# Optimization experiments

Measured on AMD Instinct MI355X. Metric: run time of the kernel, lower is better.

The kernel has to match this reference:

```python
import jax, jax.numpy as jnp
import numpy as np

B, C, O, H, W = 4, 64, 64, 128, 128
KH = KW = 3
K = KH * KW  # 9 kernel positions
MRM = 10.0   # max_residue_magnitude


def setup_inputs() -> dict:
    key = jax.random.key(0)
    ks = jax.random.split(key, 6)
    return {
        "x_main": jax.random.normal(ks[0], (B, C, H, W), jnp.float32),
        "x_extra": jax.random.normal(ks[1], (B, C, H, W), jnp.float32),
        "pre_offset": jax.random.normal(ks[2], (B, K, H, W, 2), jnp.float32) * 2.0,
        "pre_sim": jax.random.uniform(ks[3], (B, K, H, W), jnp.float32),
        "weight": jax.random.normal(ks[4], (O, C, KH, KW), jnp.float32) / np.sqrt(C * K),
        "bias": jnp.zeros((O,), jnp.float32),
        "w_om": jax.random.normal(ks[5], (3 * K, C, KH, KW), jnp.float32) * 0.01,
        "b_om": jnp.zeros((3 * K,), jnp.float32),
    }


def _bilinear(img, py, px):
    """img: [C,Hi,Wi]; py, px: [K,Ho,Wo] float sample coords. Zero padding outside."""
    Hi, Wi = img.shape[1], img.shape[2]
    y0 = jnp.floor(py)
    x0 = jnp.floor(px)
    dy = py - y0  # [K,Ho,Wo]
    dx = px - x0

    def gather(yi, xi):
        valid = ((yi >= 0) & (yi <= Hi - 1) & (xi >= 0) & (xi <= Wi - 1)).astype(img.dtype)
        yc = jnp.clip(yi, 0, Hi - 1).astype(jnp.int32)
        xc = jnp.clip(xi, 0, Wi - 1).astype(jnp.int32)
        return img[:, yc, xc] * valid[None]  # [C,K,Ho,Wo]

    v00 = gather(y0, x0)
    v01 = gather(y0, x0 + 1)
    v10 = gather(y0 + 1, x0)
    v11 = gather(y0 + 1, x0 + 1)
    return (v00 * (1 - dy) * (1 - dx) + v01 * (1 - dy) * dx
            + v10 * dy * (1 - dx) + v11 * dy * dx)


def reference(x_main, x_extra, pre_offset, pre_sim, weight, bias, w_om, b_om):
    # conv_offset_mask: 3x3, stride 1, pad 1 -> [B, 3K, H, W]
    out = jax.lax.conv_general_dilated(
        x_extra, w_om, (1, 1), ((1, 1), (1, 1)),
        dimension_numbers=("NCHW", "OIHW", "NCHW")) + b_om[None, :, None, None]
    o1, o2, mask = jnp.split(out, 3, axis=1)  # each [B,K,H,W]
    offset = MRM * jnp.tanh(jnp.concatenate([o1, o2], axis=1))  # [B,2K,H,W]
    # pre_offset reorder: even channels <- pre_offset[...,1] (y), odd <- pre_offset[...,0] (x)
    off_y = offset[:, 0::2] + pre_offset[..., 1]  # [B,K,H,W]
    off_x = offset[:, 1::2] + pre_offset[..., 0]
    mask = jax.nn.sigmoid(mask * pre_sim)  # use_sim=True

    f32 = offset.dtype
    ky = (jnp.arange(K) // KW).astype(f32)  # kernel row per position k
    kx = (jnp.arange(K) % KW).astype(f32)   # kernel col per position k
    # base grid: p = out_pos*stride - pad + k*dil = h - 1 + ky (stride=1,pad=1,dil=1)
    py = off_y + (jnp.arange(H, dtype=f32)[None, None, :, None] - 1.0) + ky[None, :, None, None]
    px = off_x + (jnp.arange(W, dtype=f32)[None, None, None, :] - 1.0) + kx[None, :, None, None]

    sampled = jax.vmap(_bilinear)(x_main, py, px)      # [B,C,K,H,W]
    sampled = sampled * mask[:, None]                   # modulated (DCNv2)
    y = jnp.einsum("bckhw,ock->bohw", sampled, weight.reshape(O, C, K))
    return y + bias[None, :, None, None]
```

## Files before the change

kernel.cpp:

```cpp
#include <hip/hip_runtime.h>
#include <math.h>

#define Bn 4
#define Cn 64
#define On 64
#define Hn 128
#define Wn 128
#define Kn 9
#define HWn (Hn*Wn)
#define ZROW 16384
#define XBSTRIDE (16385*64)

typedef short v8s __attribute__((ext_vector_type(8)));
typedef _Float16 v8h __attribute__((ext_vector_type(8)));
typedef float v4f __attribute__((ext_vector_type(4)));

__device__ inline unsigned short f2bf(float f) {
  unsigned u = __builtin_bit_cast(unsigned, f);
  u += 0x7fff + ((u >> 16) & 1);
  return (unsigned short)(u >> 16);
}
__device__ inline float bf2f(unsigned short h) {
  unsigned u = ((unsigned)h) << 16;
  return __builtin_bit_cast(float, u);
}
__device__ inline unsigned short f2h(float f) {
  _Float16 h = (_Float16)f;
  return __builtin_bit_cast(unsigned short, h);
}
__device__ inline float h2f(unsigned v) {
  _Float16 h = __builtin_bit_cast(_Float16, (unsigned short)(v & 0xffff));
  return (float)h;
}

__global__ __launch_bounds__(256) void k_prep(
    const float* __restrict__ x_main,
    const float* __restrict__ x_extra,
    const float* __restrict__ weight,
    const float* __restrict__ w_om,
    unsigned short* __restrict__ xT,
    _Float16* __restrict__ xeF,
    unsigned short* __restrict__ Wfrag,
    _Float16* __restrict__ WOMfrag)
{
  const int blk = blockIdx.x;
  const int t = threadIdx.x;
  const int lane = t & 63;
  const int grp = t >> 6;

  if (blk < 2048) {
    __shared__ float tile[64 * 65];
    int isExtra = blk >> 10;
    int b  = (blk >> 8) & 3;
    int p0 = (blk & 255) << 6;
    const float* src = (isExtra ? x_extra : x_main) + b * Cn * HWn + p0;
    #pragma unroll
    for (int i = 0; i < 16; ++i) {
      int c = i * 4 + grp;
      tile[c * 65 + lane] = src[c * HWn + lane];
    }
    __syncthreads();
    if (!isExtra) {
      unsigned short* dst = xT + b * XBSTRIDE + p0 * 64;
      #pragma unroll
      for (int i = 0; i < 16; ++i) {
        int p = i * 4 + grp;
        dst[p * 64 + lane] = f2bf(tile[lane * 65 + p]);
      }
    } else {
      _Float16* dst = xeF + b * XBSTRIDE + p0 * 64;
      #pragma unroll
      for (int i = 0; i < 16; ++i) {
        int p = i * 4 + grp;
        dst[p * 64 + lane] = (_Float16)tile[lane * 65 + p];
      }
    }
  } else {
    int rb = blk - 2048;
    for (int idx = rb * 256 + t; idx < 36864; idx += 64 * 256) {
      int j  = idx & 7;
      int ln = (idx >> 3) & 63;
      int hk = (idx >> 9) & 1;
      int ot = (idx >> 10) & 3;
      int k  = idx >> 12;
      int o = ot * 16 + (ln & 15);
      int c = hk * 32 + (ln >> 4) * 8 + j;
      Wfrag[idx] = f2bf(weight[(o * Cn + c) * Kn + k]);
    }
    for (int idx = rb * 256 + t; idx < 18432; idx += 64 * 256) {
      int j    = idx & 7;
      int ln   = (idx >> 3) & 63;
      int jt   = (idx >> 9) & 1;
      int half = (idx >> 10) & 1;
      int k9   = idx >> 11;
      int jo = jt * 16 + (ln & 15);
      int c  = half * 32 + (ln >> 4) * 8 + j;
      float v = (jo < 27) ? w_om[(jo * Cn + c) * Kn + k9] : 0.f;
      WOMfrag[idx] = (_Float16)v;
    }
    if (rb == 0 && t < 256) {
      int b = t >> 6, c = t & 63;
      xT[b * XBSTRIDE + ZROW * 64 + c] = 0;
      xeF[b * XBSTRIDE + ZROW * 64 + c] = (_Float16)0.f;
    }
  }
}

__global__ __launch_bounds__(256, 4) void k_fused(
    const unsigned short* __restrict__ xT,
    const _Float16* __restrict__ xeF,
    const unsigned short* __restrict__ Wfrag,
    const _Float16* __restrict__ WOMfrag,
    const float* __restrict__ pre_offset,
    const float* __restrict__ pre_sim,
    const float* __restrict__ b_om,
    const float* __restrict__ bias,
    float* __restrict__ out)
{
  __shared__ float jbuf[4 * 16 * 36];
  __shared__ uint4 recbuf[4 * 16 * 9];

  const int t    = threadIdx.x;
  const int lane = t & 63;
  const int wv   = __builtin_amdgcn_readfirstlane(t >> 6);
  const int blk  = blockIdx.x;
  const int b    = blk >> 8;
  const int h    = (blk >> 1) & 127;
  const int wq   = (blk & 1) * 4 + wv;
  const int kq   = lane >> 4;
  const int n    = lane & 15;
  const int w    = wq * 16 + n;

  unsigned tapoff[9];
  #pragma unroll
  for (int k9 = 0; k9 < 9; ++k9) {
    int r  = h - 1 + k9 / 3;
    int cc = w - 1 + k9 % 3;
    bool v = ((unsigned)r < (unsigned)Hn) & ((unsigned)cc < (unsigned)Wn);
    tapoff[k9] = (v ? (unsigned)(r * Wn + cc) : (unsigned)ZROW) * 64u;
  }

  const _Float16* xe = xeF + b * XBSTRIDE;
  const v8h* Wom = (const v8h*)WOMfrag;
  v4f ca0 = {0,0,0,0}, ca1 = {0,0,0,0};
  for (int k9 = 0; k9 < 9; ++k9) {
    #pragma unroll
    for (int half = 0; half < 2; ++half) {
      int abase = ((k9 * 2 + half) * 2) * 64 + lane;
      v8h A0 = Wom[abase];
      v8h A1 = Wom[abase + 64];
      v8h Bt = *(const v8h*)(xe + tapoff[k9] + half * 32 + kq * 8);
      ca0 = __builtin_amdgcn_mfma_f32_16x16x32_f16(A0, Bt, ca0, 0, 0, 0);
      ca1 = __builtin_amdgcn_mfma_f32_16x16x32_f16(A1, Bt, ca1, 0, 0, 0);
    }
  }

  float* jb = jbuf + wv * (16 * 36);
  *(v4f*)(jb + n * 36 + kq * 4)      = ca0;
  *(v4f*)(jb + n * 36 + 16 + kq * 4) = ca1;

  uint4* rb = recbuf + wv * (16 * 9);
  if (kq < 3) {
    #pragma unroll
    for (int kk = 0; kk < 3; ++kk) {
      int k = kq * 3 + kk;
      float sy = jb[n * 36 + 2 * k]     + b_om[2 * k];
      float sx = jb[n * 36 + 2 * k + 1] + b_om[2 * k + 1];
      float sm = jb[n * 36 + 18 + k]    + b_om[18 + k];
      int pbase = ((b * Kn + k) * Hn + h) * Wn + w;
      float2 po = *(const float2*)(pre_offset + pbase * 2);
      float py = 10.f * tanhf(sy) + po.y + (float)(h - 1 + k / 3);
      float px = 10.f * tanhf(sx) + po.x + (float)(w - 1 + k % 3);
      float m  = 1.f / (1.f + expf(-sm * pre_sim[pbase]));
      float fy = floorf(py), fx = floorf(px);
      float dy = py - fy, dx = px - fx;
      int y0 = (int)fy, x0 = (int)fx;
      int y1 = y0 + 1, x1 = x0 + 1;
      bool vy0 = (y0 >= 0) & (y0 < Hn), vy1 = (y1 >= 0) & (y1 < Hn);
      bool vx0 = (x0 >= 0) & (x0 < Wn), vx1 = (x1 >= 0) & (x1 < Wn);
      unsigned r00 = (vy0 & vx0) ? (unsigned)(y0 * Wn + x0) : ZROW;
      unsigned r01 = (vy0 & vx1) ? (unsigned)(y0 * Wn + x1) : ZROW;
      unsigned r10 = (vy1 & vx0) ? (unsigned)(y1 * Wn + x0) : ZROW;
      unsigned r11 = (vy1 & vx1) ? (unsigned)(y1 * Wn + x1) : ZROW;
      float wy0 = 1.f - dy, wx0 = 1.f - dx;
      uint4 rec;
      rec.x = r00 | (r01 << 16);
      rec.y = r10 | (r11 << 16);
      rec.z = (unsigned)f2h(wy0 * wx0 * m) | ((unsigned)f2h(wy0 * dx * m) << 16);
      rec.w = (unsigned)f2h(dy * wx0 * m) | ((unsigned)f2h(dy * dx * m) << 16);
      rb[n * 9 + k] = rec;
    }
  }

  v4f acc0 = {0,0,0,0}, acc1 = {0,0,0,0}, acc2 = {0,0,0,0}, acc3 = {0,0,0,0};
  const unsigned short* xb = xT + b * XBSTRIDE;
  const v8s* Wf = (const v8s*)Wfrag;

  uint4 rec0   = rb[n * 9 + 0];
  uint4 rec_nx = rb[n * 9 + 1];
  float w00 = h2f(rec0.z), w01 = h2f(rec0.z >> 16);
  float w10 = h2f(rec0.w), w11 = h2f(rec0.w >> 16);
  unsigned o00 = (rec0.x & 0xffff) * 64 + kq * 8;
  unsigned o01 = (rec0.x >> 16)    * 64 + kq * 8;
  unsigned o10 = (rec0.y & 0xffff) * 64 + kq * 8;
  unsigned o11 = (rec0.y >> 16)    * 64 + kq * 8;
  v8s C0 = *(const v8s*)(xb + o00);
  v8s C1 = *(const v8s*)(xb + o01);
  v8s C2 = *(const v8s*)(xb + o10);
  v8s C3 = *(const v8s*)(xb + o11);

  #pragma unroll
  for (int k = 0; k < 9; ++k) {
    v8s H0 = *(const v8s*)(xb + o00 + 32);
    v8s H1 = *(const v8s*)(xb + o01 + 32);
    v8s H2 = *(const v8s*)(xb + o10 + 32);
    v8s H3 = *(const v8s*)(xb + o11 + 32);

    v8s N0, N1, N2, N3;
    float nw00 = 0.f, nw01 = 0.f, nw10 = 0.f, nw11 = 0.f;
    unsigned p00 = 0, p01 = 0, p10 = 0, p11 = 0;
    if (k < 8) {
      nw00 = h2f(rec_nx.z); nw01 = h2f(rec_nx.z >> 16);
      nw10 = h2f(rec_nx.w); nw11 = h2f(rec_nx.w >> 16);
      p00 = (rec_nx.x & 0xffff) * 64 + kq * 8;
      p01 = (rec_nx.x >> 16)    * 64 + kq * 8;
      p10 = (rec_nx.y & 0xffff) * 64 + kq * 8;
      p11 = (rec_nx.y >> 16)    * 64 + kq * 8;
      N0 = *(const v8s*)(xb + p00);
      N1 = *(const v8s*)(xb + p01);
      N2 = *(const v8s*)(xb + p10);
      N3 = *(const v8s*)(xb + p11);
    }
    uint4 rec_nx2 = rec_nx;
    if (k < 7) rec_nx2 = rb[n * 9 + k + 2];

    __builtin_amdgcn_sched_barrier(0);

    const v8s* wk = Wf + (k * 8) * 64 + lane;
    v8s A0 = wk[0 * 64], A1 = wk[1 * 64], A2 = wk[2 * 64], A3 = wk[3 * 64];
    v8s A4 = wk[4 * 64], A5 = wk[5 * 64], A6 = wk[6 * 64], A7 = wk[7 * 64];

    v8s Bf0, Bf1;
    #pragma unroll
    for (int j = 0; j < 8; ++j) {
      float s = fmaf(bf2f((unsigned short)C0[j]), w00,
                fmaf(bf2f((unsigned short)C1[j]), w01,
                fmaf(bf2f((unsigned short)C2[j]), w10,
                     bf2f((unsigned short)C3[j]) * w11)));
      Bf0[j] = (short)f2bf(s);
    }
    #pragma unroll
    for (int j = 0; j < 8; ++j) {
      float s = fmaf(bf2f((unsigned short)H0[j]), w00,
                fmaf(bf2f((unsigned short)H1[j]), w01,
                fmaf(bf2f((unsigned short)H2[j]), w10,
                     bf2f((unsigned short)H3[j]) * w11)));
      Bf1[j] = (short)f2bf(s);
    }

    acc0 = __builtin_amdgcn_mfma_f32_16x16x32_bf16(A0, Bf0, acc0, 0, 0, 0);
    acc1 = __builtin_amdgcn_mfma_f32_16x16x32_bf16(A2, Bf0, acc1, 0, 0, 0);
    acc2 = __builtin_amdgcn_mfma_f32_16x16x32_bf16(A4, Bf0, acc2, 0, 0, 0);
    acc3 = __builtin_amdgcn_mfma_f32_16x16x32_bf16(A6, Bf0, acc3, 0, 0, 0);
    acc0 = __builtin_amdgcn_mfma_f32_16x16x32_bf16(A1, Bf1, acc0, 0, 0, 0);
    acc1 = __builtin_amdgcn_mfma_f32_16x16x32_bf16(A3, Bf1, acc1, 0, 0, 0);
    acc2 = __builtin_amdgcn_mfma_f32_16x16x32_bf16(A5, Bf1, acc2, 0, 0, 0);
    acc3 = __builtin_amdgcn_mfma_f32_16x16x32_bf16(A7, Bf1, acc3, 0, 0, 0);

    if (k < 8) {
      C0 = N0; C1 = N1; C2 = N2; C3 = N3;
      w00 = nw00; w01 = nw01; w10 = nw10; w11 = nw11;
      o00 = p00; o01 = p01; o10 = p10; o11 = p11;
      rec_nx = rec_nx2;
    }
  }

  const float4* b4 = (const float4*)bias;
  float4 vb0 = b4[0 * 4 + kq], vb1 = b4[1 * 4 + kq];
  float4 vb2 = b4[2 * 4 + kq], vb3 = b4[3 * 4 + kq];
  float* ob = out + (b * On) * HWn + h * Wn + wq * 16 + n;
  #pragma unroll
  for (int reg = 0; reg < 4; ++reg) {
    ob[(0 * 16 + kq * 4 + reg) * HWn] = acc0[reg] + ((const float*)&vb0)[reg];
    ob[(1 * 16 + kq * 4 + reg) * HWn] = acc1[reg] + ((const float*)&vb1)[reg];
    ob[(2 * 16 + kq * 4 + reg) * HWn] = acc2[reg] + ((const float*)&vb2)[reg];
    ob[(3 * 16 + kq * 4 + reg) * HWn] = acc3[reg] + ((const float*)&vb3)[reg];
  }
}

extern "C" void kernel_launch(void* const* d_in, const int* in_sizes, int n_in,
                              void* d_out, int out_size, void* d_ws, size_t ws_size,
                              hipStream_t stream) {
  const float* x_main     = (const float*)d_in[0];
  const float* x_extra    = (const float*)d_in[1];
  const float* pre_offset = (const float*)d_in[2];
  const float* pre_sim    = (const float*)d_in[3];
  const float* weight     = (const float*)d_in[4];
  const float* bias       = (const float*)d_in[5];
  const float* w_om       = (const float*)d_in[6];
  const float* b_om       = (const float*)d_in[7];
  float* out = (float*)d_out;

  char* ws = (char*)d_ws;
  unsigned short* xT      = (unsigned short*)(ws);
  _Float16*       xeF     = (_Float16*)(ws + 8389120);
  unsigned short* Wfrag   = (unsigned short*)(ws + 16778240);
  _Float16*       WOMfrag = (_Float16*)(ws + 16851968);

  k_prep<<<2112, 256, 0, stream>>>(x_main, x_extra, weight, w_om,
                                   xT, xeF, Wfrag, WOMfrag);
  k_fused<<<1024, 256, 0, stream>>>(xT, xeF, Wfrag, WOMfrag,
                                    pre_offset, pre_sim, b_om, bias, out);
}
```

Baseline: 150.0 us.

## Switch deformable sampling to fp16 packed math, vectorize prep, remap blocks

```diff
diff --git a/kernel.cpp b/kernel.cpp
--- a/kernel.cpp
+++ b/kernel.cpp
@@ -11,42 +11,31 @@
 #define ZROW 16384
 #define XBSTRIDE (16385*64)
 
-typedef short v8s __attribute__((ext_vector_type(8)));
 typedef _Float16 v8h __attribute__((ext_vector_type(8)));
+typedef _Float16 v2h __attribute__((ext_vector_type(2)));
 typedef float v4f __attribute__((ext_vector_type(4)));
 
-__device__ inline unsigned short f2bf(float f) {
-  unsigned u = __builtin_bit_cast(unsigned, f);
-  u += 0x7fff + ((u >> 16) & 1);
-  return (unsigned short)(u >> 16);
-}
-__device__ inline float bf2f(unsigned short h) {
-  unsigned u = ((unsigned)h) << 16;
-  return __builtin_bit_cast(float, u);
-}
 __device__ inline unsigned short f2h(float f) {
   _Float16 h = (_Float16)f;
   return __builtin_bit_cast(unsigned short, h);
 }
-__device__ inline float h2f(unsigned v) {
-  _Float16 h = __builtin_bit_cast(_Float16, (unsigned short)(v & 0xffff));
-  return (float)h;
-}
+__device__ inline _Float16 u2h(unsigned v) {
+  return __builtin_bit_cast(_Float16, (unsigned short)(v & 0xffff));
+}
+__device__ inline v8h sp8(_Float16 x) { v8h v = {x,x,x,x,x,x,x,x}; return v; }
 
 __global__ __launch_bounds__(256) void k_prep(
     const float* __restrict__ x_main,
     const float* __restrict__ x_extra,
     const float* __restrict__ weight,
     const float* __restrict__ w_om,
-    unsigned short* __restrict__ xT,
+    _Float16* __restrict__ xT,
     _Float16* __restrict__ xeF,
-    unsigned short* __restrict__ Wfrag,
+    _Float16* __restrict__ Wfrag,
     _Float16* __restrict__ WOMfrag)
 {
   const int blk = blockIdx.x;
   const int t = threadIdx.x;
-  const int lane = t & 63;
-  const int grp = t >> 6;
 
   if (blk < 2048) {
     __shared__ float tile[64 * 65];
@@ -55,25 +44,23 @@
     int p0 = (blk & 255) << 6;
     const float* src = (isExtra ? x_extra : x_main) + b * Cn * HWn + p0;
     #pragma unroll
-    for (int i = 0; i < 16; ++i) {
-      int c = i * 4 + grp;
-      tile[c * 65 + lane] = src[c * HWn + lane];
+    for (int i = 0; i < 4; ++i) {
+      int c  = i * 16 + (t >> 4);
+      int p4 = (t & 15) * 4;
+      float4 v = *(const float4*)(src + c * HWn + p4);
+      tile[c * 65 + p4 + 0] = v.x;
+      tile[c * 65 + p4 + 1] = v.y;
+      tile[c * 65 + p4 + 2] = v.z;
+      tile[c * 65 + p4 + 3] = v.w;
     }
     __syncthreads();
-    if (!isExtra) {
-      unsigned short* dst = xT + b * XBSTRIDE + p0 * 64;
-      #pragma unroll
-      for (int i = 0; i < 16; ++i) {
-        int p = i * 4 + grp;
-        dst[p * 64 + lane] = f2bf(tile[lane * 65 + p]);
-      }
-    } else {
-      _Float16* dst = xeF + b * XBSTRIDE + p0 * 64;
-      #pragma unroll
-      for (int i = 0; i < 16; ++i) {
-        int p = i * 4 + grp;
-        dst[p * 64 + lane] = (_Float16)tile[lane * 65 + p];
-      }
+    _Float16* dst = (isExtra ? xeF : xT) + b * XBSTRIDE + p0 * 64;
+    #pragma unroll
+    for (int i = 0; i < 8; ++i) {
+      int p  = i * 8 + (t >> 5);
+      int c2 = (t & 31) * 2;
+      v2h pk = { (_Float16)tile[c2 * 65 + p], (_Float16)tile[(c2 + 1) * 65 + p] };
+      *(v2h*)(dst + p * 64 + c2) = pk;
     }
   } else {
     int rb = blk - 2048;
@@ -85,7 +72,7 @@
       int k  = idx >> 12;
       int o = ot * 16 + (ln & 15);
       int c = hk * 32 + (ln >> 4) * 8 + j;
-      Wfrag[idx] = f2bf(weight[(o * Cn + c) * Kn + k]);
+      Wfrag[idx] = (_Float16)weight[(o * Cn + c) * Kn + k];
     }
     for (int idx = rb * 256 + t; idx < 18432; idx += 64 * 256) {
       int j    = idx & 7;
@@ -100,16 +87,16 @@
     }
     if (rb == 0 && t < 256) {
       int b = t >> 6, c = t & 63;
-      xT[b * XBSTRIDE + ZROW * 64 + c] = 0;
+      xT[b * XBSTRIDE + ZROW * 64 + c] = (_Float16)0.f;
       xeF[b * XBSTRIDE + ZROW * 64 + c] = (_Float16)0.f;
     }
   }
 }
 
 __global__ __launch_bounds__(256, 4) void k_fused(
-    const unsigned short* __restrict__ xT,
+    const _Float16* __restrict__ xT,
     const _Float16* __restrict__ xeF,
-    const unsigned short* __restrict__ Wfrag,
+    const _Float16* __restrict__ Wfrag,
     const _Float16* __restrict__ WOMfrag,
     const float* __restrict__ pre_offset,
     const float* __restrict__ pre_sim,
@@ -123,7 +110,8 @@
   const int t    = threadIdx.x;
   const int lane = t & 63;
   const int wv   = __builtin_amdgcn_readfirstlane(t >> 6);
-  const int blk  = blockIdx.x;
+  const int raw  = blockIdx.x;
+  const int blk  = ((raw & 7) << 7) | (raw >> 3);
   const int b    = blk >> 8;
   const int h    = (blk >> 1) & 127;
   const int wq   = (blk & 1) * 4 + wv;
@@ -169,9 +157,11 @@
       float sm = jb[n * 36 + 18 + k]    + b_om[18 + k];
       int pbase = ((b * Kn + k) * Hn + h) * Wn + w;
       float2 po = *(const float2*)(pre_offset + pbase * 2);
-      float py = 10.f * tanhf(sy) + po.y + (float)(h - 1 + k / 3);
-      float px = 10.f * tanhf(sx) + po.x + (float)(w - 1 + k % 3);
-      float m  = 1.f / (1.f + expf(-sm * pre_sim[pbase]));
+      float ey = __expf(2.f * sy);
+      float ex = __expf(2.f * sx);
+      float py = 10.f - 20.f / (ey + 1.f) + po.y + (float)(h - 1 + k / 3);
+      float px = 10.f - 20.f / (ex + 1.f) + po.x + (float)(w - 1 + k % 3);
+      float m  = 1.f / (1.f + __expf(-sm * pre_sim[pbase]));
       float fy = floorf(py), fx = floorf(px);
       float dy = py - fy, dx = px - fx;
       int y0 = (int)fy, x0 = (int)fx;
@@ -193,84 +183,64 @@
   }
 
   v4f acc0 = {0,0,0,0}, acc1 = {0,0,0,0}, acc2 = {0,0,0,0}, acc3 = {0,0,0,0};
-  const unsigned short* xb = xT + b * XBSTRIDE;
-  const v8s* Wf = (const v8s*)Wfrag;
+  const _Float16* xb = xT + b * XBSTRIDE;
+  const v8h* Wf = (const v8h*)Wfrag;
 
   uint4 rec0   = rb[n * 9 + 0];
   uint4 rec_nx = rb[n * 9 + 1];
-  float w00 = h2f(rec0.z), w01 = h2f(rec0.z >> 16);
-  float w10 = h2f(rec0.w), w11 = h2f(rec0.w >> 16);
-  unsigned o00 = (rec0.x & 0xffff) * 64 + kq * 8;
-  unsigned o01 = (rec0.x >> 16)    * 64 + kq * 8;
-  unsigned o10 = (rec0.y & 0xffff) * 64 + kq * 8;
-  unsigned o11 = (rec0.y >> 16)    * 64 + kq * 8;
-  v8s C0 = *(const v8s*)(xb + o00);
-  v8s C1 = *(const v8s*)(xb + o01);
-  v8s C2 = *(const v8s*)(xb + o10);
-  v8s C3 = *(const v8s*)(xb + o11);
+  _Float16 h00 = u2h(rec0.z), h01 = u2h(rec0.z >> 16);
+  _Float16 h10 = u2h(rec0.w), h11 = u2h(rec0.w >> 16);
+  unsigned o00 = (rec0.x & 0xffff) * 64u + kq * 8;
+  unsigned o01 = (rec0.x >> 16)    * 64u + kq * 8;
+  unsigned o10 = (rec0.y & 0xffff) * 64u + kq * 8;
+  unsigned o11 = (rec0.y >> 16)    * 64u + kq * 8;
+  v8h C0 = *(const v8h*)(xb + o00), D0 = *(const v8h*)(xb + o00 + 32);
+  v8h C1 = *(const v8h*)(xb + o01), D1 = *(const v8h*)(xb + o01 + 32);
+  v8h C2 = *(const v8h*)(xb + o10), D2 = *(const v8h*)(xb + o10 + 32);
+  v8h C3 = *(const v8h*)(xb + o11), D3 = *(const v8h*)(xb + o11 + 32);
 
   #pragma unroll
   for (int k = 0; k < 9; ++k) {
-    v8s H0 = *(const v8s*)(xb + o00 + 32);
-    v8s H1 = *(const v8s*)(xb + o01 + 32);
-    v8s H2 = *(const v8s*)(xb + o10 + 32);
-    v8s H3 = *(const v8s*)(xb + o11 + 32);
-
-    v8s N0, N1, N2, N3;
-    float nw00 = 0.f, nw01 = 0.f, nw10 = 0.f, nw11 = 0.f;
-    unsigned p00 = 0, p01 = 0, p10 = 0, p11 = 0;
+    v8h N0, N1, N2, N3, M0, M1, M2, M3;
+    _Float16 nh00 = (_Float16)0.f, nh01 = (_Float16)0.f;
+    _Float16 nh10 = (_Float16)0.f, nh11 = (_Float16)0.f;
     if (k < 8) {
-      nw00 = h2f(rec_nx.z); nw01 = h2f(rec_nx.z >> 16);
-      nw10 = h2f(rec_nx.w); nw11 = h2f(rec_nx.w >> 16);
-      p00 = (rec_nx.x & 0xffff) * 64 + kq * 8;
-      p01 = (rec_nx.x >> 16)    * 64 + kq * 8;
-      p10 = (rec_nx.y & 0xffff) * 64 + kq * 8;
-      p11 = (rec_nx.y >> 16)    * 64 + kq * 8;
-      N0 = *(const v8s*)(xb + p00);
-      N1 = *(const v8s*)(xb + p01);
-      N2 = *(const v8s*)(xb + p10);
-      N3 = *(const v8s*)(xb + p11);
+      nh00 = u2h(rec_nx.z); nh01 = u2h(rec_nx.z >> 16);
+      nh10 = u2h(rec_nx.w); nh11 = u2h(rec_nx.w >> 16);
+      unsigned p00 = (rec_nx.x & 0xffff) * 64u + kq * 8;
+      unsigned p01 = (rec_nx.x >> 16)    * 64u + kq * 8;
+      unsigned p10 = (rec_nx.y & 0xffff) * 64u + kq * 8;
+      unsigned p11 = (rec_nx.y >> 16)    * 64u + kq * 8;
+      N0 = *(const v8h*)(xb + p00); M0 = *(const v8h*)(xb + p00 + 32);
+      N1 = *(const v8h*)(xb + p01); M1 = *(const v8h*)(xb + p01 + 32);
+      N2 = *(const v8h*)(xb + p10); M2 = *(const v8h*)(xb + p10 + 32);
+      N3 = *(const v8h*)(xb + p11); M3 = *(const v8h*)(xb + p11 + 32);
     }
     uint4 rec_nx2 = rec_nx;
     if (k < 7) rec_nx2 = rb[n * 9 + k + 2];
 
     __builtin_amdgcn_sched_barrier(0);
 
-    const v8s* wk = Wf + (k * 8) * 64 + lane;
-    v8s A0 = wk[0 * 64], A1 = wk[1 * 64], A2 = wk[2 * 64], A3 = wk[3 * 64];
-    v8s A4 = wk[4 * 64], A5 = wk[5 * 64], A6 = wk[6 * 64], A7 = wk[7 * 64];
-
-    v8s Bf0, Bf1;
-    #pragma unroll
-    for (int j = 0; j < 8; ++j) {
-      float s = fmaf(bf2f((unsigned short)C0[j]), w00,
-                fmaf(bf2f((unsigned short)C1[j]), w01,
-                fmaf(bf2f((unsigned short)C2[j]), w10,
-                     bf2f((unsigned short)C3[j]) * w11)));
-      Bf0[j] = (short)f2bf(s);
-    }
-    #pragma unroll
-    for (int j = 0; j < 8; ++j) {
-      float s = fmaf(bf2f((unsigned short)H0[j]), w00,
-                fmaf(bf2f((unsigned short)H1[j]), w01,
-                fmaf(bf2f((unsigned short)H2[j]), w10,
-                     bf2f((unsigned short)H3[j]) * w11)));
-      Bf1[j] = (short)f2bf(s);
-    }
-
-    acc0 = __builtin_amdgcn_mfma_f32_16x16x32_bf16(A0, Bf0, acc0, 0, 0, 0);
-    acc1 = __builtin_amdgcn_mfma_f32_16x16x32_bf16(A2, Bf0, acc1, 0, 0, 0);
-    acc2 = __builtin_amdgcn_mfma_f32_16x16x32_bf16(A4, Bf0, acc2, 0, 0, 0);
-    acc3 = __builtin_amdgcn_mfma_f32_16x16x32_bf16(A6, Bf0, acc3, 0, 0, 0);
-    acc0 = __builtin_amdgcn_mfma_f32_16x16x32_bf16(A1, Bf1, acc0, 0, 0, 0);
-    acc1 = __builtin_amdgcn_mfma_f32_16x16x32_bf16(A3, Bf1, acc1, 0, 0, 0);
-    acc2 = __builtin_amdgcn_mfma_f32_16x16x32_bf16(A5, Bf1, acc2, 0, 0, 0);
-    acc3 = __builtin_amdgcn_mfma_f32_16x16x32_bf16(A7, Bf1, acc3, 0, 0, 0);
+    const v8h* wk = Wf + (k * 8) * 64 + lane;
+    v8h A0 = wk[0 * 64], A1 = wk[1 * 64], A2 = wk[2 * 64], A3 = wk[3 * 64];
+    v8h A4 = wk[4 * 64], A5 = wk[5 * 64], A6 = wk[6 * 64], A7 = wk[7 * 64];
+
+    v8h Bf0 = C0 * sp8(h00) + C1 * sp8(h01) + C2 * sp8(h10) + C3 * sp8(h11);
+    v8h Bf1 = D0 * sp8(h00) + D1 * sp8(h01) + D2 * sp8(h10) + D3 * sp8(h11);
+
+    acc0 = __builtin_amdgcn_mfma_f32_16x16x32_f16(A0, Bf0, acc0, 0, 0, 0);
+    acc1 = __builtin_amdgcn_mfma_f32_16x16x32_f16(A2, Bf0, acc1, 0, 0, 0);
+    acc2 = __builtin_amdgcn_mfma_f32_16x16x32_f16(A4, Bf0, acc2, 0, 0, 0);
+    acc3 = __builtin_amdgcn_mfma_f32_16x16x32_f16(A6, Bf0, acc3, 0, 0, 0);
+    acc0 = __builtin_amdgcn_mfma_f32_16x16x32_f16(A1, Bf1, acc0, 0, 0, 0);
+    acc1 = __builtin_amdgcn_mfma_f32_16x16x32_f16(A3, Bf1, acc1, 0, 0, 0);
+    acc2 = __builtin_amdgcn_mfma_f32_16x16x32_f16(A5, Bf1, acc2, 0, 0, 0);
+    acc3 = __builtin_amdgcn_mfma_f32_16x16x32_f16(A7, Bf1, acc3, 0, 0, 0);
 
     if (k < 8) {
       C0 = N0; C1 = N1; C2 = N2; C3 = N3;
-      w00 = nw00; w01 = nw01; w10 = nw10; w11 = nw11;
-      o00 = p00; o01 = p01; o10 = p10; o11 = p11;
+      D0 = M0; D1 = M1; D2 = M2; D3 = M3;
+      h00 = nh00; h01 = nh01; h10 = nh10; h11 = nh11;
       rec_nx = rec_nx2;
     }
   }
@@ -302,10 +272,10 @@
   float* out = (float*)d_out;
 
   char* ws = (char*)d_ws;
-  unsigned short* xT      = (unsigned short*)(ws);
-  _Float16*       xeF     = (_Float16*)(ws + 8389120);
-  unsigned short* Wfrag   = (unsigned short*)(ws + 16778240);
-  _Float16*       WOMfrag = (_Float16*)(ws + 16851968);
+  _Float16* xT      = (_Float16*)(ws);
+  _Float16* xeF     = (_Float16*)(ws + 8389120);
+  _Float16* Wfrag   = (_Float16*)(ws + 16778240);
+  _Float16* WOMfrag = (_Float16*)(ws + 16851968);
 
   k_prep<<<2112, 256, 0, stream>>>(x_main, x_extra, weight, w_om,
                                    xT, xeF, Wfrag, WOMfrag);
```

Result: slower. 164.9 us (+9.9%).
